# Kernel tuning notes

Measured on AMD Instinct MI355X. Metric: run time of the kernel, lower is better.

Reference implementation:

```python
import jax, jax.numpy as jnp
import numpy as np

B, NQ, NK = 4, 2048, 2048
DQ, DK, DV, H = 256, 256, 256, 4
DH = DV // H
EPS = 1e-5


def _layernorm(x, g, b):
    m = jnp.mean(x, axis=-1, keepdims=True)
    v = jnp.mean(jnp.square(x - m), axis=-1, keepdims=True)
    return (x - m) * jax.lax.rsqrt(v + EPS) * g + b


def setup_inputs() -> dict:
    key = jax.random.key(0)
    ks = jax.random.split(key, 12)
    s = lambda d: 1.0 / np.sqrt(d)
    return {
        "Q": jax.random.normal(ks[0], (B, NQ, DQ), jnp.float32),
        "K": jax.random.normal(ks[1], (B, NK, DK), jnp.float32),
        "Wq": jax.random.uniform(ks[2], (DQ, DV), jnp.float32, -s(DQ), s(DQ)),
        "bq": jnp.zeros((DV,), jnp.float32),
        "Wk": jax.random.uniform(ks[3], (DK, DV), jnp.float32, -s(DK), s(DK)),
        "bk": jnp.zeros((DV,), jnp.float32),
        "Wv": jax.random.uniform(ks[4], (DK, DV), jnp.float32, -s(DK), s(DK)),
        "bv": jnp.zeros((DV,), jnp.float32),
        "W1": jax.random.uniform(ks[5], (DV, DV), jnp.float32, -s(DV), s(DV)),
        "b1": jnp.zeros((DV,), jnp.float32),
        "W2": jax.random.uniform(ks[6], (DV, DV), jnp.float32, -s(DV), s(DV)),
        "b2": jnp.zeros((DV,), jnp.float32),
        "g0": jnp.ones((DV,), jnp.float32),
        "beta0": jnp.zeros((DV,), jnp.float32),
        "g1": jnp.ones((DV,), jnp.float32),
        "beta1": jnp.zeros((DV,), jnp.float32),
    }


def reference(Q, K, Wq, bq, Wk, bk, Wv, bv, W1, b1, W2, b2, g0, beta0, g1, beta1):
    Qp = (Q @ Wq + bq).reshape(B, NQ, H, DH)  # split last dim into heads
    Kp = (K @ Wk + bk).reshape(B, NK, H, DH)
    Vp = (K @ Wv + bv).reshape(B, NK, H, DH)
    scale = 1.0 / np.sqrt(DH)  # K_.size(-1)**0.5 after head split
    scores = jnp.einsum("bqhd,bkhd->bhqk", Qp, Kp) * scale
    attn = jax.nn.softmax(scores, axis=-1)
    out = jnp.einsum("bhqk,bkhd->bqhd", attn, Vp)
    O = (Qp + out).reshape(B, NQ, DV)  # residual with projected Q, heads re-concat
    O = _layernorm(O, g0, beta0)
    ffn = jax.nn.relu(O @ W1 + b1) @ W2 + b2
    return _layernorm(O + ffn, g1, beta1)
```

## Files before the change

kernel.cpp:

```cpp
#include <hip/hip_runtime.h>


typedef float fx4 __attribute__((ext_vector_type(4)));
typedef short short8 __attribute__((ext_vector_type(8)));
typedef short shortx4 __attribute__((ext_vector_type(4)));
typedef unsigned int uint2v __attribute__((ext_vector_type(2)));
typedef unsigned int uint4v __attribute__((ext_vector_type(4)));

#define BB  4
#define NN  2048
#define DD  256
#define HH  4
#define DHH 64

__device__ __forceinline__ float bf2f(unsigned short u) {
    union { unsigned int i; float f; } v; v.i = ((unsigned int)u) << 16; return v.f;
}
__device__ __forceinline__ unsigned short f2bf(float f) {
    union { float f; unsigned int i; } v; v.f = f;
    unsigned int r = v.i + 0x7FFF + ((v.i >> 16) & 1);
    return (unsigned short)(r >> 16);
}
__device__ __forceinline__ unsigned int fbits(float f) {
    union { float f; unsigned int i; } v; v.f = f; return v.i;
}
__device__ __forceinline__ unsigned int packbf(float lo, float hi) {
    unsigned int a = fbits(lo), b = fbits(hi);
    a = (a + 0x7FFF + ((a >> 16) & 1)) >> 16;
    b = (b + 0x7FFF + ((b >> 16) & 1)) & 0xFFFF0000u;
    return a | b;
}

__global__ __launch_bounds__(256) void wt_prep(
        const float* __restrict__ w0, const float* __restrict__ w1,
        const float* __restrict__ w2, const float* __restrict__ w3,
        const float* __restrict__ w4, unsigned short* __restrict__ dst) {
    __shared__ unsigned short T[64 * 73];
    const int tid = threadIdx.x;
    const int z = blockIdx.z;
    const float* W = (z == 0) ? w0 : (z == 1) ? w1 : (z == 2) ? w2 : (z == 3) ? w3 : w4;
    unsigned short* WT = dst + z * 65536;
    const int nb = blockIdx.x * 64, kb = blockIdx.y * 64;
    {
        int kl = tid >> 2, c0 = (tid & 3) * 16;
        const float* src = W + (size_t)(kb + kl) * DD + nb + c0;
#pragma unroll
        for (int i = 0; i < 16; ++i) T[kl * 73 + c0 + i] = f2bf(src[i]);
    }
    __syncthreads();
    {
        int nl = tid >> 2, k0 = (tid & 3) * 16;
        short8 o0, o1;
#pragma unroll
        for (int i = 0; i < 8; ++i) {
            o0[i] = (short)T[(k0 + i) * 73 + nl];
            o1[i] = (short)T[(k0 + 8 + i) * 73 + nl];
        }
        short8* d = (short8*)(WT + (size_t)(nb + nl) * DD + kb + k0);
        d[0] = o0; d[1] = o1;
    }
}

template<int LAYOUT>
__device__ __forceinline__ void gemm32_body(
        const float* __restrict__ Ain, const unsigned short* __restrict__ WT,
        const float* __restrict__ bias, unsigned short* __restrict__ Cout, int bx) {
    __shared__ unsigned short As[32 * 264];
    const int tid = threadIdx.x;
    const int lane = tid & 63, w = tid >> 6;
    const int l15 = lane & 15, quad = lane >> 4;
    const int r0 = (bx >> 1) * 32;
    const int c0w = (bx & 1) * 128 + w * 32;
    short8 wf[8][2];
#pragma unroll
    for (int kc = 0; kc < 8; ++kc)
#pragma unroll
        for (int dt = 0; dt < 2; ++dt)
            wf[kc][dt] = *(const short8*)(WT + (size_t)(c0w + dt * 16 + l15) * DD + kc * 32 + 8 * quad);
    fx4 bb[2];
    float bv[2];
#pragma unroll
    for (int dt = 0; dt < 2; ++dt) {
        if (LAYOUT == 2) bv[dt] = bias[c0w + dt * 16 + l15];
        else             bb[dt] = *(const fx4*)(bias + c0w + dt * 16 + 4 * quad);
    }
    {
        int row = tid >> 3, c0 = (tid & 7) * 32;
        short8 o[4];
        const fx4* s4 = (const fx4*)(Ain + (size_t)(r0 + row) * DD + c0);
#pragma unroll
        for (int j = 0; j < 4; ++j) {
            fx4 v0 = s4[2 * j], v1 = s4[2 * j + 1];
#pragma unroll
            for (int i = 0; i < 4; ++i) {
                o[j][i]     = (short)f2bf(v0[i]);
                o[j][i + 4] = (short)f2bf(v1[i]);
            }
        }
        short8* d = (short8*)(As + row * 264 + c0);
#pragma unroll
        for (int j = 0; j < 4; ++j) d[j] = o[j];
    }
    __syncthreads();
    fx4 acc[2][2];
#pragma unroll
    for (int mt = 0; mt < 2; ++mt)
#pragma unroll
        for (int dt = 0; dt < 2; ++dt) acc[mt][dt] = (fx4){0.f, 0.f, 0.f, 0.f};
#pragma unroll
    for (int kc = 0; kc < 8; ++kc) {
        short8 a0 = *(const short8*)(As + l15 * 264 + kc * 32 + 8 * quad);
        short8 a1 = *(const short8*)(As + (16 + l15) * 264 + kc * 32 + 8 * quad);
#pragma unroll
        for (int dt = 0; dt < 2; ++dt) {
            if (LAYOUT == 2) {
                acc[0][dt] = __builtin_amdgcn_mfma_f32_16x16x32_bf16(a0, wf[kc][dt], acc[0][dt], 0, 0, 0);
                acc[1][dt] = __builtin_amdgcn_mfma_f32_16x16x32_bf16(a1, wf[kc][dt], acc[1][dt], 0, 0, 0);
            } else {
                acc[0][dt] = __builtin_amdgcn_mfma_f32_16x16x32_bf16(wf[kc][dt], a0, acc[0][dt], 0, 0, 0);
                acc[1][dt] = __builtin_amdgcn_mfma_f32_16x16x32_bf16(wf[kc][dt], a1, acc[1][dt], 0, 0, 0);
            }
        }
    }
    if (LAYOUT == 0) {
#pragma unroll
        for (int mt = 0; mt < 2; ++mt) {
            const size_t grow = r0 + mt * 16 + l15;
#pragma unroll
            for (int dt = 0; dt < 2; ++dt) {
                shortx4 pk;
#pragma unroll
                for (int r = 0; r < 4; ++r) pk[r] = (short)f2bf(acc[mt][dt][r] + bb[dt][r]);
                *(shortx4*)(Cout + grow * DD + c0w + dt * 16 + 4 * quad) = pk;
            }
        }
    } else if (LAYOUT == 1) {
        const int tl = (r0 & 2047) >> 5;
        const int b  = r0 >> 11;
#pragma unroll
        for (int mt = 0; mt < 2; ++mt) {
            const int key32 = mt * 16 + l15;
#pragma unroll
            for (int dt = 0; dt < 2; ++dt) {
                const int col = c0w + dt * 16 + 4 * quad;
                shortx4 pk;
#pragma unroll
                for (int r = 0; r < 4; ++r) pk[r] = (short)f2bf(acc[mt][dt][r] + bb[dt][r]);
                unsigned short* dstp = Cout
                    + ((size_t)((b * 4 + (col >> 6)) * 64 + tl)) * 2048
                    + ((col >> 5) & 1) * 1024 + key32 * 32 + (col & 31);
                *(shortx4*)dstp = pk;
            }
        }
    } else {
        const int tl = (r0 & 2047) >> 5;
        const int b  = r0 >> 11;
#pragma unroll
        for (int mt = 0; mt < 2; ++mt) {
#pragma unroll
            for (int dt = 0; dt < 2; ++dt) {
                const int col = c0w + dt * 16 + l15;
                shortx4 pk;
#pragma unroll
                for (int r = 0; r < 4; ++r) pk[r] = (short)f2bf(acc[mt][dt][r] + bv[dt]);
                unsigned short* dstp = Cout
                    + ((size_t)((b * 4 + (col >> 6)) * 64 + tl)) * 2048
                    + (col & 63) * 32 + mt * 16 + 4 * quad;
                *(shortx4*)dstp = pk;
            }
        }
    }
}

__global__ __launch_bounds__(256, 4) void qkv_mfma(
        const float* __restrict__ Q, const float* __restrict__ K,
        const unsigned short* __restrict__ WT5,
        const float* __restrict__ bq, const float* __restrict__ bk,
        const float* __restrict__ bv,
        unsigned short* __restrict__ Qp, unsigned short* __restrict__ KT,
        unsigned short* __restrict__ VT2) {
    const int z = blockIdx.y;
    if (z == 0)      gemm32_body<0>(Q, WT5,           bq, Qp,  blockIdx.x);
    else if (z == 1) gemm32_body<1>(K, WT5 + 65536,   bk, KT,  blockIdx.x);
    else             gemm32_body<2>(K, WT5 + 131072,  bv, VT2, blockIdx.x);
}

__global__ __launch_bounds__(256, 2) void attn_mfma(
        const unsigned short* __restrict__ Qp, const unsigned short* __restrict__ KT,
        const unsigned short* __restrict__ VT2, float* __restrict__ Od,
        float* __restrict__ Lp) {
    __shared__ unsigned short kbuf[2][2048];
    __shared__ unsigned short vbuf[2][2048];
    __shared__ unsigned int pbuf[4][256];
    const int tid = threadIdx.x;
    const int lane = tid & 63, w = tid >> 6;
    const int l15 = lane & 15, quad = lane >> 4;
    const int gb = blockIdx.x;
    const int bh = ((gb & 7) << 1) | ((gb >> 10) & 1);
    const int qc = (gb >> 3) & 31;
    const int kq = (gb >> 8) & 3;
    const int h  = bh & 3;
    const int b  = bh >> 2;
    const int qrow = qc * 64 + w * 16;
    const int sw = 4 * ((l15 >> 1) & 3);

    short8 aq0, aq1;
    {
        const unsigned short* qptr = Qp + ((size_t)(b * NN + qrow + l15) * DD + h * DHH + 8 * quad);
        aq0 = *(const short8*)qptr;
        aq1 = *(const short8*)(qptr + 32);
    }
    fx4 od0 = (fx4){0.f, 0.f, 0.f, 0.f};
    fx4 od1 = (fx4){0.f, 0.f, 0.f, 0.f};
    fx4 od2 = (fx4){0.f, 0.f, 0.f, 0.f};
    fx4 od3 = (fx4){0.f, 0.f, 0.f, 0.f};
    float lsum = 0.0f;

    unsigned int* pw = &pbuf[w][0];
    const int wcol = (2 * quad) ^ sw;
    const int rcol = (4 * quad) ^ sw;
    const unsigned short* ktb = KT  + (size_t)(bh * 64 + kq * 16) * 2048 + tid * 8;
    const unsigned short* vtb = VT2 + (size_t)(bh * 64 + kq * 16) * 2048 + tid * 8;
    const int ew = (tid * 8) ^ (((tid >> 3) & 3) << 3);
    const int fo = (l15 * 32 + 8 * quad) ^ (((l15 >> 1) & 3) << 3);

    {
        uint4v kr = *(const uint4v*)ktb;
        uint4v vr = *(const uint4v*)vtb;
        *(uint4v*)&kbuf[0][ew] = kr;
        *(uint4v*)&vbuf[0][ew] = vr;
    }
    __syncthreads();

    for (int t = 0; t < 16; ++t) {
        const int cur = t & 1;
        const int tn = (t < 15) ? t + 1 : 15;
        uint4v kr = *(const uint4v*)(ktb + (size_t)tn * 2048);
        uint4v vr = *(const uint4v*)(vtb + (size_t)tn * 2048);

        const unsigned short* kb = &kbuf[cur][fo];
        short8 ck0 = *(const short8*)(kb);
        short8 ck1 = *(const short8*)(kb + 1024);
        short8 ck2 = *(const short8*)(kb + 512);
        short8 ck3 = *(const short8*)(kb + 1536);
        const unsigned short* vb = &vbuf[cur][fo];
        short8 cv0 = *(const short8*)(vb);
        short8 cv1 = *(const short8*)(vb + 512);
        short8 cv2 = *(const short8*)(vb + 1024);
        short8 cv3 = *(const short8*)(vb + 1536);

        const fx4 z_ = (fx4){0.f, 0.f, 0.f, 0.f};
        fx4 s0 = __builtin_amdgcn_mfma_f32_16x16x32_bf16(ck0, aq0, z_, 0, 0, 0);
        s0     = __builtin_amdgcn_mfma_f32_16x16x32_bf16(ck1, aq1, s0, 0, 0, 0);
        fx4 s1 = __builtin_amdgcn_mfma_f32_16x16x32_bf16(ck2, aq0, z_, 0, 0, 0);
        s1     = __builtin_amdgcn_mfma_f32_16x16x32_bf16(ck3, aq1, s1, 0, 0, 0);
        s0[0] = __expf(s0[0] * 0.125f); s0[1] = __expf(s0[1] * 0.125f);
        s0[2] = __expf(s0[2] * 0.125f); s0[3] = __expf(s0[3] * 0.125f);
        s1[0] = __expf(s1[0] * 0.125f); s1[1] = __expf(s1[1] * 0.125f);
        s1[2] = __expf(s1[2] * 0.125f); s1[3] = __expf(s1[3] * 0.125f);
        lsum += s0[0] + s0[1] + s0[2] + s0[3];
        lsum += s1[0] + s1[1] + s1[2] + s1[3];
        uint2v w1_ = (uint2v){packbf(s0[0], s0[1]), packbf(s0[2], s0[3])};
        uint2v w2_ = (uint2v){packbf(s1[0], s1[1]), packbf(s1[2], s1[3])};
        *(uint2v*)(pw + l15 * 16 + wcol)       = w1_;
        *(uint2v*)(pw + l15 * 16 + (wcol ^ 8)) = w2_;
        short8 bp = *(const short8*)(pw + l15 * 16 + rcol);
        od0 = __builtin_amdgcn_mfma_f32_16x16x32_bf16(cv0, bp, od0, 0, 0, 0);
        od1 = __builtin_amdgcn_mfma_f32_16x16x32_bf16(cv1, bp, od1, 0, 0, 0);
        od2 = __builtin_amdgcn_mfma_f32_16x16x32_bf16(cv2, bp, od2, 0, 0, 0);
        od3 = __builtin_amdgcn_mfma_f32_16x16x32_bf16(cv3, bp, od3, 0, 0, 0);

        *(uint4v*)&kbuf[cur ^ 1][ew] = kr;
        *(uint4v*)&vbuf[cur ^ 1][ew] = vr;
        __syncthreads();
    }

    lsum += __shfl_xor(lsum, 16);
    lsum += __shfl_xor(lsum, 32);
    const size_t grow = (size_t)(b * NN) + qrow + l15;
    float* obase = Od + (size_t)kq * 2097152 + grow * DD + h * DHH;
    *(fx4*)(obase + 0 * 16 + 4 * quad) = od0;
    *(fx4*)(obase + 1 * 16 + 4 * quad) = od1;
    *(fx4*)(obase + 2 * 16 + 4 * quad) = od2;
    *(fx4*)(obase + 3 * 16 + 4 * quad) = od3;
    if (quad == 0) Lp[(size_t)kq * 32768 + grow * 4 + h] = lsum;
}

__global__ __launch_bounds__(512) void ffn1_fused(
        const float* __restrict__ Od, const float* __restrict__ Lp,
        const unsigned short* __restrict__ Qp,
        const float* __restrict__ g, const float* __restrict__ be,
        const unsigned short* __restrict__ WT1, const float* __restrict__ b1,
        float* __restrict__ O, unsigned short* __restrict__ H1) {
    __shared__ unsigned short As[32 * 264];
    const int tid = threadIdx.x;
    const int lane = tid & 63, w = tid >> 6;
    const int l15 = lane & 15, quad = lane >> 4;
    const int r0 = blockIdx.x * 32;
    const int c0w = w * 32;
    {
        const int row = tid >> 4, c0 = (tid & 15) * 16;
        const size_t grow = r0 + row;
        const int hh = c0 >> 6;
        const float inv = 1.0f / (Lp[grow * 4 + hh] + Lp[32768 + grow * 4 + hh]
                                + Lp[65536 + grow * 4 + hh] + Lp[98304 + grow * 4 + hh]);
        float v[16];
        float s1 = 0.f, s2 = 0.f;
        const float* odp = Od + grow * DD + c0;
#pragma unroll
        for (int j = 0; j < 4; ++j) {
            fx4 m0 = *(const fx4*)(odp + j * 4);
            fx4 m1 = *(const fx4*)(odp + 2097152 + j * 4);
            fx4 m2 = *(const fx4*)(odp + 4194304 + j * 4);
            fx4 m3 = *(const fx4*)(odp + 6291456 + j * 4);
            shortx4 qv = *(const shortx4*)(Qp + grow * DD + c0 + j * 4);
#pragma unroll
            for (int i = 0; i < 4; ++i) {
                float x = (m0[i] + m1[i] + m2[i] + m3[i]) * inv
                        + bf2f((unsigned short)qv[i]);
                v[j * 4 + i] = x; s1 += x; s2 += x * x;
            }
        }
        s1 += __shfl_xor(s1, 1); s2 += __shfl_xor(s2, 1);
        s1 += __shfl_xor(s1, 2); s2 += __shfl_xor(s2, 2);
        s1 += __shfl_xor(s1, 4); s2 += __shfl_xor(s2, 4);
        s1 += __shfl_xor(s1, 8); s2 += __shfl_xor(s2, 8);
        const float mean = s1 * (1.0f / 256.0f);
        const float var  = s2 * (1.0f / 256.0f) - mean * mean;
        const float rstd = rsqrtf(var + 1e-5f);
#pragma unroll
        for (int j = 0; j < 4; ++j) {
            fx4 gg = *(const fx4*)(g + c0 + j * 4);
            fx4 ee = *(const fx4*)(be + c0 + j * 4);
            fx4 o; shortx4 ob;
#pragma unroll
            for (int i = 0; i < 4; ++i) {
                o[i] = (v[j * 4 + i] - mean) * rstd * gg[i] + ee[i];
                ob[i] = (short)f2bf(o[i]);
            }
            *(fx4*)(O + grow * DD + c0 + j * 4) = o;
            *(shortx4*)(As + row * 264 + c0 + j * 4) = ob;
        }
    }
    short8 wf[8][2];
#pragma unroll
    for (int kc = 0; kc < 8; ++kc)
#pragma unroll
        for (int dt = 0; dt < 2; ++dt)
            wf[kc][dt] = *(const short8*)(WT1 + (size_t)(c0w + dt * 16 + l15) * DD + kc * 32 + 8 * quad);
    fx4 bb[2];
#pragma unroll
    for (int dt = 0; dt < 2; ++dt)
        bb[dt] = *(const fx4*)(b1 + c0w + dt * 16 + 4 * quad);
    __syncthreads();
    fx4 acc[2][2];
#pragma unroll
    for (int mt = 0; mt < 2; ++mt)
#pragma unroll
        for (int dt = 0; dt < 2; ++dt) acc[mt][dt] = (fx4){0.f, 0.f, 0.f, 0.f};
#pragma unroll
    for (int kc = 0; kc < 8; ++kc) {
        short8 a0 = *(const short8*)(As + l15 * 264 + kc * 32 + 8 * quad);
        short8 a1 = *(const short8*)(As + (16 + l15) * 264 + kc * 32 + 8 * quad);
#pragma unroll
        for (int dt = 0; dt < 2; ++dt) {
            acc[0][dt] = __builtin_amdgcn_mfma_f32_16x16x32_bf16(wf[kc][dt], a0, acc[0][dt], 0, 0, 0);
            acc[1][dt] = __builtin_amdgcn_mfma_f32_16x16x32_bf16(wf[kc][dt], a1, acc[1][dt], 0, 0, 0);
        }
    }
#pragma unroll
    for (int mt = 0; mt < 2; ++mt) {
        const size_t grow = r0 + mt * 16 + l15;
#pragma unroll
        for (int dt = 0; dt < 2; ++dt) {
            shortx4 pk;
#pragma unroll
            for (int r = 0; r < 4; ++r)
                pk[r] = (short)f2bf(fmaxf(acc[mt][dt][r] + bb[dt][r], 0.0f));
            *(shortx4*)(H1 + grow * DD + c0w + dt * 16 + 4 * quad) = pk;
        }
    }
}

__global__ __launch_bounds__(512, 4) void gemm_ffn2_ln(
        const unsigned short* __restrict__ Ain, const unsigned short* __restrict__ WT,
        const float* __restrict__ bias, const float* __restrict__ R,
        const float* __restrict__ g, const float* __restrict__ be,
        float* __restrict__ out) {
    __shared__ unsigned short As[16 * 264];
    __shared__ float lnb[2][8][16];
    const int tid = threadIdx.x;
    const int lane = tid & 63, w = tid >> 6;
    const int l15 = lane & 15, quad = lane >> 4;
    const int r0 = blockIdx.x * 16;
    const int c0w = w * 32;
    short8 wf[8][2];
#pragma unroll
    for (int kc = 0; kc < 8; ++kc)
#pragma unroll
        for (int dt = 0; dt < 2; ++dt)
            wf[kc][dt] = *(const short8*)(WT + (size_t)(c0w + dt * 16 + l15) * DD + kc * 32 + 8 * quad);
    fx4 bb[2], gg[2], ee[2];
#pragma unroll
    for (int dt = 0; dt < 2; ++dt) {
        int col = c0w + dt * 16 + 4 * quad;
        bb[dt] = *(const fx4*)(bias + col);
        gg[dt] = *(const fx4*)(g + col);
        ee[dt] = *(const fx4*)(be + col);
    }
    {
        int row = tid >> 5, c0 = (tid & 31) * 8;
        *(short8*)(As + row * 264 + c0) = *(const short8*)(Ain + (size_t)(r0 + row) * DD + c0);
    }
    __syncthreads();
    fx4 acc[2];
#pragma unroll
    for (int i = 0; i < 2; ++i) acc[i] = (fx4){0.f, 0.f, 0.f, 0.f};
#pragma unroll
    for (int kc = 0; kc < 8; ++kc) {
        short8 a = *(const short8*)(As + l15 * 264 + kc * 32 + 8 * quad);
#pragma unroll
        for (int dt = 0; dt < 2; ++dt)
            acc[dt] = __builtin_amdgcn_mfma_f32_16x16x32_bf16(wf[kc][dt], a, acc[dt], 0, 0, 0);
    }
    const size_t grow = r0 + l15;
    fx4 v4[2];
    float p1 = 0.f, p2 = 0.f;
#pragma unroll
    for (int dt = 0; dt < 2; ++dt) {
        fx4 rv = *(const fx4*)(R + grow * DD + c0w + dt * 16 + 4 * quad);
#pragma unroll
        for (int r = 0; r < 4; ++r) {
            float x = acc[dt][r] + bb[dt][r] + rv[r];
            v4[dt][r] = x; p1 += x; p2 += x * x;
        }
    }
    p1 += __shfl_xor(p1, 16); p2 += __shfl_xor(p2, 16);
    p1 += __shfl_xor(p1, 32); p2 += __shfl_xor(p2, 32);
    if (quad == 0) { lnb[0][w][l15] = p1; lnb[1][w][l15] = p2; }
    __syncthreads();
    float s1 = 0.f, s2 = 0.f;
#pragma unroll
    for (int ww = 0; ww < 8; ++ww) { s1 += lnb[0][ww][l15]; s2 += lnb[1][ww][l15]; }
    const float mean = s1 * (1.0f / 256.0f);
    const float var  = s2 * (1.0f / 256.0f) - mean * mean;
    const float rstd = rsqrtf(var + 1e-5f);
#pragma unroll
    for (int dt = 0; dt < 2; ++dt) {
        fx4 o;
#pragma unroll
        for (int r = 0; r < 4; ++r)
            o[r] = (v4[dt][r] - mean) * rstd * gg[dt][r] + ee[dt][r];
        *(fx4*)(out + grow * DD + c0w + dt * 16 + 4 * quad) = o;
    }
}

extern "C" void kernel_launch(void* const* d_in, const int* in_sizes, int n_in,
                              void* d_out, int out_size, void* d_ws, size_t ws_size,
                              hipStream_t stream) {
    (void)in_sizes; (void)n_in; (void)out_size; (void)ws_size;
    const float* Q     = (const float*)d_in[0];
    const float* K     = (const float*)d_in[1];
    const float* Wq    = (const float*)d_in[2];
    const float* bq    = (const float*)d_in[3];
    const float* Wk    = (const float*)d_in[4];
    const float* bk    = (const float*)d_in[5];
    const float* Wv    = (const float*)d_in[6];
    const float* bv    = (const float*)d_in[7];
    const float* W1    = (const float*)d_in[8];
    const float* b1    = (const float*)d_in[9];
    const float* W2    = (const float*)d_in[10];
    const float* b2    = (const float*)d_in[11];
    const float* g0    = (const float*)d_in[12];
    const float* beta0 = (const float*)d_in[13];
    const float* g1    = (const float*)d_in[14];
    const float* beta1 = (const float*)d_in[15];

    char* ws = (char*)d_ws;
    unsigned short* Qp  = (unsigned short*)(ws);
    unsigned short* KT  = (unsigned short*)(ws + (4u  << 20));
    unsigned short* VT2 = (unsigned short*)(ws + (8u  << 20));
    float*          Od  = (float*)(ws + (12u << 20));
    float*          O   = (float*)(ws + (44u << 20));
    float*          Lp  = (float*)(ws + (52u << 20));
    unsigned short* WT5 = (unsigned short*)(ws + (53u << 20));
    unsigned short* H1  = Qp;
    float*          out = (float*)d_out;

    const unsigned short* WT1 = WT5 + 3 * 65536;
    const unsigned short* WT2 = WT5 + 4 * 65536;

    const int M = BB * NN;

    wt_prep<<<dim3(4, 4, 5), 256, 0, stream>>>(Wq, Wk, Wv, W1, W2, WT5);
    qkv_mfma<<<dim3(M / 16, 3), 256, 0, stream>>>(Q, K, WT5, bq, bk, bv, Qp, KT, VT2);
    attn_mfma<<<2048, 256, 0, stream>>>(Qp, KT, VT2, Od, Lp);
    ffn1_fused<<<M / 32, 512, 0, stream>>>(Od, Lp, Qp, g0, beta0, WT1, b1, O, H1);
    gemm_ffn2_ln<<<M / 16, 512, 0, stream>>>(H1, WT2, b2, O, g1, beta1, out);
}
```

Measured before the change: 170.7 us.

## Fuse FFN second GEMM and final layernorm into the FFN1 kernel

Merges the FFN2 GEMM plus residual-add layernorm into the FFN1 kernel. The ReLU hidden activations now stay in shared memory instead of being written to and re-read from global memory, and one kernel launch disappears. In exchange the fused kernel uses more shared memory and registers, since it holds a second set of weight fragments. Each block also handles 32 rows instead of 16 in the FFN2 stage, which halves the grid for that stage.

```diff
diff --git a/kernel.cpp b/kernel.cpp
--- a/kernel.cpp
+++ b/kernel.cpp
@@ -286,13 +286,17 @@
     if (quad == 0) Lp[(size_t)kq * 32768 + grow * 4 + h] = lsum;
 }
 
-__global__ __launch_bounds__(512) void ffn1_fused(
+__global__ __launch_bounds__(512) void ffn_fused(
         const float* __restrict__ Od, const float* __restrict__ Lp,
         const unsigned short* __restrict__ Qp,
-        const float* __restrict__ g, const float* __restrict__ be,
+        const float* __restrict__ g0, const float* __restrict__ be0,
         const unsigned short* __restrict__ WT1, const float* __restrict__ b1,
-        float* __restrict__ O, unsigned short* __restrict__ H1) {
+        const unsigned short* __restrict__ WT2, const float* __restrict__ b2,
+        const float* __restrict__ g1, const float* __restrict__ be1,
+        float* __restrict__ O, float* __restrict__ out) {
     __shared__ unsigned short As[32 * 264];
+    __shared__ unsigned short Hs[32 * 264];
+    __shared__ float lnb[2][8][32];
     const int tid = threadIdx.x;
     const int lane = tid & 63, w = tid >> 6;
     const int l15 = lane & 15, quad = lane >> 4;
@@ -330,8 +334,8 @@
         const float rstd = rsqrtf(var + 1e-5f);
 #pragma unroll
         for (int j = 0; j < 4; ++j) {
-            fx4 gg = *(const fx4*)(g + c0 + j * 4);
-            fx4 ee = *(const fx4*)(be + c0 + j * 4);
+            fx4 gg = *(const fx4*)(g0 + c0 + j * 4);
+            fx4 ee = *(const fx4*)(be0 + c0 + j * 4);
             fx4 o; shortx4 ob;
 #pragma unroll
             for (int i = 0; i < 4; ++i) {
@@ -348,10 +352,10 @@
 #pragma unroll
         for (int dt = 0; dt < 2; ++dt)
             wf[kc][dt] = *(const short8*)(WT1 + (size_t)(c0w + dt * 16 + l15) * DD + kc * 32 + 8 * quad);
-    fx4 bb[2];
+    fx4 bb1[2];
 #pragma unroll
     for (int dt = 0; dt < 2; ++dt)
-        bb[dt] = *(const fx4*)(b1 + c0w + dt * 16 + 4 * quad);
+        bb1[dt] = *(const fx4*)(b1 + c0w + dt * 16 + 4 * quad);
     __syncthreads();
     fx4 acc[2][2];
 #pragma unroll
@@ -370,88 +374,82 @@
     }
 #pragma unroll
     for (int mt = 0; mt < 2; ++mt) {
-        const size_t grow = r0 + mt * 16 + l15;
 #pragma unroll
         for (int dt = 0; dt < 2; ++dt) {
             shortx4 pk;
 #pragma unroll
             for (int r = 0; r < 4; ++r)
-                pk[r] = (short)f2bf(fmaxf(acc[mt][dt][r] + bb[dt][r], 0.0f));
-            *(shortx4*)(H1 + grow * DD + c0w + dt * 16 + 4 * quad) = pk;
-        }
-    }
-}
-
-__global__ __launch_bounds__(512, 4) void gemm_ffn2_ln(
-        const unsigned short* __restrict__ Ain, const unsigned short* __restrict__ WT,
-        const float* __restrict__ bias, const float* __restrict__ R,
-        const float* __restrict__ g, const float* __restrict__ be,
-        float* __restrict__ out) {
-    __shared__ unsigned short As[16 * 264];
-    __shared__ float lnb[2][8][16];
-    const int tid = threadIdx.x;
-    const int lane = tid & 63, w = tid >> 6;
-    const int l15 = lane & 15, quad = lane >> 4;
-    const int r0 = blockIdx.x * 16;
-    const int c0w = w * 32;
-    short8 wf[8][2];
+                pk[r] = (short)f2bf(fmaxf(acc[mt][dt][r] + bb1[dt][r], 0.0f));
+            *(shortx4*)(Hs + (mt * 16 + l15) * 264 + c0w + dt * 16 + 4 * quad) = pk;
+        }
+    }
+    short8 wf2[8][2];
 #pragma unroll
     for (int kc = 0; kc < 8; ++kc)
 #pragma unroll
         for (int dt = 0; dt < 2; ++dt)
-            wf[kc][dt] = *(const short8*)(WT + (size_t)(c0w + dt * 16 + l15) * DD + kc * 32 + 8 * quad);
-    fx4 bb[2], gg[2], ee[2];
+            wf2[kc][dt] = *(const short8*)(WT2 + (size_t)(c0w + dt * 16 + l15) * DD + kc * 32 + 8 * quad);
+    fx4 bb2[2], gg1[2], ee1[2];
 #pragma unroll
     for (int dt = 0; dt < 2; ++dt) {
         int col = c0w + dt * 16 + 4 * quad;
-        bb[dt] = *(const fx4*)(bias + col);
-        gg[dt] = *(const fx4*)(g + col);
-        ee[dt] = *(const fx4*)(be + col);
-    }
-    {
-        int row = tid >> 5, c0 = (tid & 31) * 8;
-        *(short8*)(As + row * 264 + c0) = *(const short8*)(Ain + (size_t)(r0 + row) * DD + c0);
-    }
-    __syncthreads();
-    fx4 acc[2];
-#pragma unroll
-    for (int i = 0; i < 2; ++i) acc[i] = (fx4){0.f, 0.f, 0.f, 0.f};
+        bb2[dt] = *(const fx4*)(b2 + col);
+        gg1[dt] = *(const fx4*)(g1 + col);
+        ee1[dt] = *(const fx4*)(be1 + col);
+    }
+    __syncthreads();
+    fx4 acc2[2][2];
+#pragma unroll
+    for (int mt = 0; mt < 2; ++mt)
+#pragma unroll
+        for (int dt = 0; dt < 2; ++dt) acc2[mt][dt] = (fx4){0.f, 0.f, 0.f, 0.f};
 #pragma unroll
     for (int kc = 0; kc < 8; ++kc) {
-        short8 a = *(const short8*)(As + l15 * 264 + kc * 32 + 8 * quad);
-#pragma unroll
-        for (int dt = 0; dt < 2; ++dt)
-            acc[dt] = __builtin_amdgcn_mfma_f32_16x16x32_bf16(wf[kc][dt], a, acc[dt], 0, 0, 0);
-    }
-    const size_t grow = r0 + l15;
-    fx4 v4[2];
-    float p1 = 0.f, p2 = 0.f;
-#pragma unroll
-    for (int dt = 0; dt < 2; ++dt) {
-        fx4 rv = *(const fx4*)(R + grow * DD + c0w + dt * 16 + 4 * quad);
-#pragma unroll
-        for (int r = 0; r < 4; ++r) {
-            float x = acc[dt][r] + bb[dt][r] + rv[r];
-            v4[dt][r] = x; p1 += x; p2 += x * x;
-        }
-    }
-    p1 += __shfl_xor(p1, 16); p2 += __shfl_xor(p2, 16);
-    p1 += __shfl_xor(p1, 32); p2 += __shfl_xor(p2, 32);
-    if (quad == 0) { lnb[0][w][l15] = p1; lnb[1][w][l15] = p2; }
-    __syncthreads();
-    float s1 = 0.f, s2 = 0.f;
-#pragma unroll
-    for (int ww = 0; ww < 8; ++ww) { s1 += lnb[0][ww][l15]; s2 += lnb[1][ww][l15]; }
-    const float mean = s1 * (1.0f / 256.0f);
-    const float var  = s2 * (1.0f / 256.0f) - mean * mean;
-    const float rstd = rsqrtf(var + 1e-5f);
-#pragma unroll
-    for (int dt = 0; dt < 2; ++dt) {
-        fx4 o;
-#pragma unroll
-        for (int r = 0; r < 4; ++r)
-            o[r] = (v4[dt][r] - mean) * rstd * gg[dt][r] + ee[dt][r];
-        *(fx4*)(out + grow * DD + c0w + dt * 16 + 4 * quad) = o;
+        short8 a0 = *(const short8*)(Hs + l15 * 264 + kc * 32 + 8 * quad);
+        short8 a1 = *(const short8*)(Hs + (16 + l15) * 264 + kc * 32 + 8 * quad);
+#pragma unroll
+        for (int dt = 0; dt < 2; ++dt) {
+            acc2[0][dt] = __builtin_amdgcn_mfma_f32_16x16x32_bf16(wf2[kc][dt], a0, acc2[0][dt], 0, 0, 0);
+            acc2[1][dt] = __builtin_amdgcn_mfma_f32_16x16x32_bf16(wf2[kc][dt], a1, acc2[1][dt], 0, 0, 0);
+        }
+    }
+    fx4 v4[2][2];
+#pragma unroll
+    for (int mt = 0; mt < 2; ++mt) {
+        const size_t grow = r0 + mt * 16 + l15;
+        float p1 = 0.f, p2 = 0.f;
+#pragma unroll
+        for (int dt = 0; dt < 2; ++dt) {
+            fx4 rv = *(const fx4*)(O + grow * DD + c0w + dt * 16 + 4 * quad);
+#pragma unroll
+            for (int r = 0; r < 4; ++r) {
+                float x = acc2[mt][dt][r] + bb2[dt][r] + rv[r];
+                v4[mt][dt][r] = x; p1 += x; p2 += x * x;
+            }
+        }
+        p1 += __shfl_xor(p1, 16); p2 += __shfl_xor(p2, 16);
+        p1 += __shfl_xor(p1, 32); p2 += __shfl_xor(p2, 32);
+        if (quad == 0) { lnb[0][w][mt * 16 + l15] = p1; lnb[1][w][mt * 16 + l15] = p2; }
+    }
+    __syncthreads();
+#pragma unroll
+    for (int mt = 0; mt < 2; ++mt) {
+        const int row = mt * 16 + l15;
+        float s1 = 0.f, s2 = 0.f;
+#pragma unroll
+        for (int ww = 0; ww < 8; ++ww) { s1 += lnb[0][ww][row]; s2 += lnb[1][ww][row]; }
+        const float mean = s1 * (1.0f / 256.0f);
+        const float var  = s2 * (1.0f / 256.0f) - mean * mean;
+        const float rstd = rsqrtf(var + 1e-5f);
+        const size_t grow = r0 + row;
+#pragma unroll
+        for (int dt = 0; dt < 2; ++dt) {
+            fx4 o;
+#pragma unroll
+            for (int r = 0; r < 4; ++r)
+                o[r] = (v4[mt][dt][r] - mean) * rstd * gg1[dt][r] + ee1[dt][r];
+            *(fx4*)(out + grow * DD + c0w + dt * 16 + 4 * quad) = o;
+        }
     }
 }
 
@@ -484,7 +482,6 @@
     float*          O   = (float*)(ws + (44u << 20));
     float*          Lp  = (float*)(ws + (52u << 20));
     unsigned short* WT5 = (unsigned short*)(ws + (53u << 20));
-    unsigned short* H1  = Qp;
     float*          out = (float*)d_out;
 
     const unsigned short* WT1 = WT5 + 3 * 65536;
@@ -495,6 +492,6 @@
     wt_prep<<<dim3(4, 4, 5), 256, 0, stream>>>(Wq, Wk, Wv, W1, W2, WT5);
     qkv_mfma<<<dim3(M / 16, 3), 256, 0, stream>>>(Q, K, WT5, bq, bk, bv, Qp, KT, VT2);
     attn_mfma<<<2048, 256, 0, stream>>>(Qp, KT, VT2, Od, Lp);
-    ffn1_fused<<<M / 32, 512, 0, stream>>>(Od, Lp, Qp, g0, beta0, WT1, b1, O, H1);
-    gemm_ffn2_ln<<<M / 16, 512, 0, stream>>>(H1, WT2, b2, O, g1, beta1, out);
-}
+    ffn_fused<<<M / 32, 512, 0, stream>>>(Od, Lp, Qp, g0, beta0, WT1, b1,
+                                          WT2, b2, g1, beta1, O, out);
+}
```

Result: faster. 164.8 us (-3.4%).
